# Kernel optimization log

Measured on AMD Instinct MI355X. Metric: run time of the kernel, lower is better.

## Reference

```python
import jax, jax.numpy as jnp
import numpy as np

N = 50000      # nodes
E = 800000     # edges (avg degree 16)
B = 8          # graphs in batch
H = 128        # hidden (message_passer out_channels)
FF = 64        # fourier_feat_dim -> fourier features have dim 2*FF
REPEATS = 4    # repeats_training
OUT = 4        # output_dim
IN_X = 5
IN_MASK = 3

def _fourier(x, M):
    # https://arxiv.org/pdf/2106.02795.pdf : [cos(xM), sin(xM)] / sqrt(2F)
    p = x @ M
    return jnp.concatenate([jnp.cos(p), jnp.sin(p)], axis=-1) / jnp.sqrt(2.0 * M.shape[1])

def _seg_mean(v, idx, n):
    s = jax.ops.segment_sum(v, idx, num_segments=n)
    c = jax.ops.segment_sum(jnp.ones((v.shape[0],), v.dtype), idx, num_segments=n)
    return s / jnp.maximum(c, 1.0)[:, None]

def setup_inputs() -> dict:
    key = jax.random.key(0)
    ks = jax.random.split(key, 16)
    x = jax.random.normal(ks[0], (N, IN_X), jnp.float32)
    x_mask = jax.random.bernoulli(ks[1], 0.1, (N, IN_MASK)).astype(jnp.float32)
    edge_index = jax.random.randint(ks[2], (2, E), 0, N)
    edge_attr = jax.random.normal(ks[3], (E, 3), jnp.float32)
    pos = jax.random.uniform(ks[4], (N, 2), jnp.float32)
    batch = jnp.sort(jax.random.randint(ks[5], (N,), 0, B))
    sampling_points = jax.random.uniform(ks[6], (2,), jnp.float32)
    fourier_mat = jax.random.normal(ks[7], (2, FF), jnp.float32)  # learnable, init N(0,1)
    W_enc = jax.random.normal(ks[8], (IN_X + IN_MASK, H), jnp.float32) * 0.1
    b_enc = jnp.zeros((H,), jnp.float32)
    W_msg = jax.random.normal(ks[9], (2 * H + 3, H), jnp.float32) * 0.05
    b_msg = jnp.zeros((H,), jnp.float32)
    W_upd = jax.random.normal(ks[10], (4 * H, H), jnp.float32) * 0.05
    b_upd = jnp.zeros((H,), jnp.float32)
    W_dec = jax.random.normal(ks[11], (H, OUT), jnp.float32) * 0.1
    b_dec = jnp.zeros((OUT,), jnp.float32)
    return dict(x=x, x_mask=x_mask, edge_index=edge_index, edge_attr=edge_attr,
                pos=pos, batch=batch, sampling_points=sampling_points,
                fourier_mat=fourier_mat, W_enc=W_enc, b_enc=b_enc,
                W_msg=W_msg, b_msg=b_msg, W_upd=W_upd, b_upd=b_upd,
                W_dec=W_dec, b_dec=b_dec)

def reference(x, x_mask, edge_index, edge_attr, pos, batch, sampling_points,
              fourier_mat, W_enc, b_enc, W_msg, b_msg, W_upd, b_upd, W_dec, b_dec):
    bc = x_mask[:, -1]                                   # 0/1 BC flag
    x_full = jnp.concatenate([x, x_mask], axis=1)        # x = concat([x, x_mask])
    keys_ff = _fourier(pos, fourier_mat)                 # input fourier features [N, 2F]
    h = jax.nn.relu(x_full @ W_enc + b_enc)              # encoder -> [N, H]

    # x_BC: scatter-mean over BC nodes per graph (computed once)
    bc_sum = jax.ops.segment_sum(h * bc[:, None], batch, num_segments=B)
    bc_cnt = jax.ops.segment_sum(bc, batch, num_segments=B)
    x_BC = bc_sum / jnp.maximum(bc_cnt, 1.0)[:, None]    # [B, H]

    x_graph = _seg_mean(h, batch, B)                     # global_mean_pool [B, H]
    src, dst = edge_index[0], edge_index[1]
    deg = jnp.maximum(jax.ops.segment_sum(jnp.ones((E,), h.dtype), dst, num_segments=N), 1.0)

    for _ in range(REPEATS):  # repeated message passing
        m = jax.nn.relu(jnp.concatenate([h[src], h[dst], edge_attr], axis=1) @ W_msg + b_msg)
        agg = jax.ops.segment_sum(m, dst, num_segments=N) / deg[:, None]  # scatter-mean
        upd_in = jnp.concatenate([h, agg, x_graph[batch], x_BC[batch]], axis=1)
        h = h + jax.nn.relu(upd_in @ W_upd + b_upd)
        x_graph = _seg_mean(h, batch, B)                 # re-pool each repeat

    decoded = h @ W_dec + b_dec                          # [N, OUT]

    # kernelized fourier-feature interpolation at the sampling point
    q = _fourier(sampling_points, fourier_mat)           # [2F]
    nq = q / jnp.linalg.norm(q)
    nk = keys_ff / jnp.linalg.norm(keys_ff, axis=1, keepdims=True)
    vals_sum = h.sum(axis=0)                             # [H]
    kwv = nk.T @ h                                       # [2F, H]
    ks_sum = nk.sum(axis=0)                              # [2F]
    enc = (vals_sum + nq @ kwv) / (N + nq @ ks_sum)      # [H]
    U_sampled = enc @ W_dec + b_dec                      # [OUT]
    # pack (U_sampled, decoded) into one array: row 0 = sampled point, rows 1: = nodes
    return jnp.concatenate([U_sampled[None, :], decoded], axis=0)
```

## Files before the change

### kernel.cpp

```cpp
#include <hip/hip_runtime.h>
#include <math.h>

#define Nn 50000
#define Ee 800000
#define Bb 8
#define ROUNDS 4
#define KWVB 512
#define SCB 196
#define AP 40
#define HP 132
#define KS 40
#define NBK 196
#define P1B 391
#define CHUNK 2047

typedef __attribute__((ext_vector_type(8))) short bf16x8;
typedef __attribute__((ext_vector_type(4))) float f32x4;

__device__ inline short f2bf(float f) {
  union { float f; unsigned u; } v; v.f = f;
  unsigned r = v.u + 0x7fff + ((v.u >> 16) & 1);
  return (short)(r >> 16);
}
__device__ inline float bf2f(short s) {
  union { float f; unsigned u; } v; v.u = ((unsigned)(unsigned short)s) << 16;
  return v.f;
}

__global__ __launch_bounds__(256) void encode_seg(
    const float* __restrict__ x, const float* __restrict__ xm,
    const int* __restrict__ batch, const float* __restrict__ W,
    const float* __restrict__ b, float* __restrict__ h,
    float* __restrict__ gsum, float* __restrict__ gcnt,
    float* __restrict__ bcsum, float* __restrict__ bccnt) {
  __shared__ float xs5[128 * 5];
  __shared__ float xm3[128 * 3];
  __shared__ float ls[Bb * 128];
  __shared__ float lb[Bb * 128];
  __shared__ float lc[Bb], lbc[Bb];
  const int t = threadIdx.x;
  const int nBase = blockIdx.x * 128;
  const int j = t & 127, half = t >> 7;
  const int base5 = nBase * 5, base3 = nBase * 3;
  for (int q = t; q < 640; q += 256) xs5[q] = (base5 + q < Nn * 5) ? x[base5 + q] : 0.f;
  for (int q = t; q < 384; q += 256) xm3[q] = (base3 + q < Nn * 3) ? xm[base3 + q] : 0.f;
  for (int q = t; q < Bb * 128; q += 256) { ls[q] = 0.f; lb[q] = 0.f; }
  if (t < Bb) { lc[t] = 0.f; lbc[t] = 0.f; }
  float Wcol[8];
#pragma unroll
  for (int k = 0; k < 8; k++) Wcol[k] = W[k * 128 + j];
  const float bj = b[j];
  __syncthreads();
  int curb = -1;
  float runh = 0.f, runb = 0.f, runc = 0.f, runbc = 0.f;
  for (int kk = 0; kk < 64; kk++) {
    int i = nBase + kk * 2 + half;
    if (i >= Nn) break;
    int li = i - nBase;
    float acc = bj;
#pragma unroll
    for (int k = 0; k < 5; k++) acc = fmaf(xs5[li * 5 + k], Wcol[k], acc);
#pragma unroll
    for (int k = 0; k < 3; k++) acc = fmaf(xm3[li * 3 + k], Wcol[5 + k], acc);
    float v = fmaxf(acc, 0.f);
    h[(size_t)i * 128 + j] = v;
    float bc = xm3[li * 3 + 2];
    int g = batch[i];
    if (g != curb) {
      if (curb >= 0) {
        atomicAdd(&ls[curb * 128 + j], runh);
        atomicAdd(&lb[curb * 128 + j], runb);
        if (j == 0) { atomicAdd(&lc[curb], runc); atomicAdd(&lbc[curb], runbc); }
      }
      curb = g; runh = runb = runc = runbc = 0.f;
    }
    runh += v; runb += v * bc;
    if (j == 0) { runc += 1.f; runbc += bc; }
  }
  if (curb >= 0) {
    atomicAdd(&ls[curb * 128 + j], runh);
    atomicAdd(&lb[curb * 128 + j], runb);
    if (j == 0) { atomicAdd(&lc[curb], runc); atomicAdd(&lbc[curb], runbc); }
  }
  __syncthreads();
  for (int q = t; q < Bb * 128; q += 256) {
    float a = ls[q], c = lb[q];
    if (a != 0.f) atomicAdd(&gsum[q], a);
    if (c != 0.f) atomicAdd(&bcsum[q], c);
  }
  if (t < Bb) { atomicAdd(&gcnt[t], lc[t]); atomicAdd(&bccnt[t], lbc[t]); }
}

__global__ __launch_bounds__(256) void split_w_kernel(
    const float* __restrict__ Wm, const float* __restrict__ Wu,
    short* __restrict__ Wmt_h, short* __restrict__ Wmt_l,
    short* __restrict__ Wut_h, short* __restrict__ Wut_l) {
  int idx = blockIdx.x * 256 + threadIdx.x;
  if (idx < 32768) {
    int k = idx & 127, n = (idx >> 7) & 127, y = idx >> 14;
    float w = Wm[(size_t)(y * 128 + k) * 128 + n];
    short hi = f2bf(w);
    Wmt_h[idx] = hi;
    Wmt_l[idx] = f2bf(w - bf2f(hi));
  } else if (idx < 65536) {
    int j = idx - 32768;
    int k = j & 255, n = j >> 8;
    float w = Wu[(size_t)k * 128 + n];
    short hi = f2bf(w);
    Wut_h[j] = hi;
    Wut_l[j] = f2bf(w - bf2f(hi));
  }
}

__global__ __launch_bounds__(256) void bkt_cnt(const int* __restrict__ ei,
                                               int* __restrict__ bktcnt) {
  __shared__ int hist[NBK];
  int t = threadIdx.x;
  for (int q = t; q < NBK; q += 256) hist[q] = 0;
  __syncthreads();
  int base = blockIdx.x * CHUNK;
  int end = base + CHUNK < Ee ? base + CHUNK : Ee;
  for (int e = base + t; e < end; e += 256) atomicAdd(&hist[ei[Ee + e] >> 8], 1);
  __syncthreads();
  for (int q = t; q < NBK; q += 256)
    if (hist[q]) atomicAdd(&bktcnt[q], hist[q]);
}
__global__ __launch_bounds__(256) void bkt_scan(const int* __restrict__ bktcnt,
                                                int* __restrict__ bktbase,
                                                int* __restrict__ bktcur) {
  __shared__ int s[256];
  int t = threadIdx.x;
  int v = (t < NBK) ? bktcnt[t] : 0;
  s[t] = v;
  __syncthreads();
  for (int off = 1; off < 256; off <<= 1) {
    int x = (t >= off) ? s[t - off] : 0;
    __syncthreads();
    s[t] += x;
    __syncthreads();
  }
  int ex = s[t] - v;
  if (t < NBK) { bktbase[t] = ex; bktcur[t] = ex; }
  if (t == NBK - 1) bktbase[NBK] = ex + v;
}
__global__ __launch_bounds__(256) void bkt_part(
    const int* __restrict__ ei, const float* __restrict__ ea,
    int* __restrict__ bktcur, int2* __restrict__ recA,
    unsigned char* __restrict__ dlo) {
  __shared__ int hist[NBK], lbase[NBK], lcur[NBK];
  int t = threadIdx.x;
  for (int q = t; q < NBK; q += 256) hist[q] = 0;
  __syncthreads();
  int base = blockIdx.x * CHUNK;
  int end = base + CHUNK < Ee ? base + CHUNK : Ee;
  for (int e = base + t; e < end; e += 256) atomicAdd(&hist[ei[Ee + e] >> 8], 1);
  __syncthreads();
  for (int q = t; q < NBK; q += 256) {
    int c = hist[q];
    lbase[q] = c ? atomicAdd(&bktcur[q], c) : 0;
    lcur[q] = 0;
  }
  __syncthreads();
  for (int e = base + t; e < end; e += 256) {
    int d = ei[Ee + e];
    int bk = d >> 8;
    int p = lbase[bk] + atomicAdd(&lcur[bk], 1);
    unsigned r0 = (unsigned)ei[e] |
                  ((unsigned)(unsigned short)f2bf(ea[3 * (size_t)e + 0]) << 16);
    unsigned r1 = (unsigned)(unsigned short)f2bf(ea[3 * (size_t)e + 1]) |
                  ((unsigned)(unsigned short)f2bf(ea[3 * (size_t)e + 2]) << 16);
    recA[p] = make_int2((int)r0, (int)r1);
    dlo[p] = (unsigned char)(d & 255);
  }
}
__global__ __launch_bounds__(256) void dst_cnt(const int* __restrict__ bktbase,
                                               const unsigned char* __restrict__ dlo,
                                               int* __restrict__ cnt) {
  __shared__ int hh[256];
  int t = threadIdx.x;
  hh[t] = 0;
  __syncthreads();
  int b = blockIdx.x;
  int lo = bktbase[b], hi = bktbase[b + 1];
  for (int i = lo + t; i < hi; i += 256) atomicAdd(&hh[dlo[i]], 1);
  __syncthreads();
  int d = b * 256 + t;
  if (d < Nn) cnt[d] = hh[t];
}
__global__ __launch_bounds__(256) void bsum_kernel(const int* __restrict__ cnt,
                                                   int* __restrict__ bsum) {
  __shared__ int wsum[4];
  int t = threadIdx.x;
  int i = blockIdx.x * 256 + t;
  int v = (i < Nn) ? cnt[i] : 0;
#pragma unroll
  for (int off = 32; off > 0; off >>= 1) v += __shfl_down(v, off);
  if ((t & 63) == 0) wsum[t >> 6] = v;
  __syncthreads();
  if (t == 0) bsum[blockIdx.x] = wsum[0] + wsum[1] + wsum[2] + wsum[3];
}
__global__ __launch_bounds__(256) void scan_top_kernel(const int* __restrict__ bsum,
                                                       int* __restrict__ boff) {
  __shared__ int s[256];
  int t = threadIdx.x;
  int v = (t < SCB) ? bsum[t] : 0;
  s[t] = v;
  __syncthreads();
  for (int off = 1; off < 256; off <<= 1) {
    int x = (t >= off) ? s[t - off] : 0;
    __syncthreads();
    s[t] += x;
    __syncthreads();
  }
  boff[t] = s[t] - v;
}
__global__ __launch_bounds__(256) void apply_kernel(
    const int* __restrict__ cnt, const int* __restrict__ boff,
    int* __restrict__ rowptr, float* __restrict__ invdeg) {
  __shared__ int s[256];
  int t = threadIdx.x;
  int i = blockIdx.x * 256 + t;
  int v = (i < Nn) ? cnt[i] : 0;
  s[t] = v;
  __syncthreads();
  for (int off = 1; off < 256; off <<= 1) {
    int x = (t >= off) ? s[t - off] : 0;
    __syncthreads();
    s[t] += x;
    __syncthreads();
  }
  int ex = boff[blockIdx.x] + s[t] - v;
  if (i < Nn) {
    rowptr[i] = ex;
    invdeg[i] = 1.0f / fmaxf((float)v, 1.0f);
    if (i == Nn - 1) rowptr[Nn] = ex + v;
  }
}
__global__ __launch_bounds__(256) void bkt_fin(
    const int* __restrict__ bktbase, const int2* __restrict__ recA,
    const unsigned char* __restrict__ dlo, const int* __restrict__ rowptr,
    int2* __restrict__ rec) {
  __shared__ int cur[256];
  int t = threadIdx.x;
  int b = blockIdx.x;
  int d = b * 256 + t;
  cur[t] = (d < Nn) ? rowptr[d] : 0;
  __syncthreads();
  int lo = bktbase[b], hi = bktbase[b + 1];
  for (int i = lo + t; i < hi; i += 256) {
    int dl = dlo[i];
    int p = atomicAdd(&cur[dl], 1);
    rec[p] = recA[i];
  }
}

__global__ __launch_bounds__(128) void gb_static_kernel(
    const float* __restrict__ bcsum, const float* __restrict__ bccnt,
    const float* __restrict__ Wu, const float* __restrict__ bu,
    float* __restrict__ gbst) {
  __shared__ float xb[128];
  int g = blockIdx.x, t = threadIdx.x;
  xb[t] = bcsum[g * 128 + t] / fmaxf(bccnt[g], 1.f);
  __syncthreads();
  float acc = bu[t];
#pragma unroll 4
  for (int k = 0; k < 128; k++) acc = fmaf(xb[k], Wu[(size_t)(384 + k) * 128 + t], acc);
  gbst[g * 128 + t] = acc;
}

__global__ __launch_bounds__(128) void gb_dyn_kernel(
    const float* __restrict__ gsum, const float* __restrict__ gcnt,
    const float* __restrict__ gbst, const float* __restrict__ Wu,
    float* __restrict__ gb) {
  __shared__ float xg[128];
  int g = blockIdx.x, t = threadIdx.x;
  xg[t] = gsum[g * 128 + t] / fmaxf(gcnt[g], 1.f);
  __syncthreads();
  float acc = gbst[g * 128 + t];
#pragma unroll 4
  for (int k = 0; k < 128; k++) acc = fmaf(xg[k], Wu[(size_t)(256 + k) * 128 + t], acc);
  gb[g * 128 + t] = acc;
}

__global__ __launch_bounds__(256) void proj_mfma(
    const float* __restrict__ h, const short* __restrict__ Wth,
    const short* __restrict__ Wtl, unsigned char* __restrict__ hs8,
    unsigned short* __restrict__ hdbf) {
  __shared__ short Ah_s[128 * AP], Al_s[128 * AP];
  __shared__ short Bh_s[128 * AP], Bl_s[128 * AP];
  const int t = threadIdx.x;
  const int nBase = blockIdx.x * 128;
  const int yoff = blockIdx.y * 16384;
  const int wave = t >> 6, lane = t & 63;
  const int ml = lane & 15, quad = lane >> 4;
  const int ko = quad * 8;

  f32x4 acc[2][8];
#pragma unroll
  for (int nt = 0; nt < 2; nt++)
#pragma unroll
    for (int mt = 0; mt < 8; mt++)
#pragma unroll
      for (int q = 0; q < 4; q++) acc[nt][mt][q] = 0.f;

  const int srow = t >> 1;
  const int kc = (t & 1) * 16;
  const int nd0 = nBase + srow;
  const int nn = nd0 < Nn ? nd0 : Nn - 1;

  for (int c = 0; c < 4; c++) {
    const float* p = &h[(size_t)nn * 128 + c * 32 + kc];
    float4 u0 = *(const float4*)(p + 0);
    float4 u1 = *(const float4*)(p + 4);
    float4 u2 = *(const float4*)(p + 8);
    float4 u3 = *(const float4*)(p + 12);
    const int k0 = c * 32;
    const bf16x8 gb0 = *(const bf16x8*)&Wth[(size_t)yoff + srow * 128 + k0 + kc];
    const bf16x8 gb1 = *(const bf16x8*)&Wth[(size_t)yoff + srow * 128 + k0 + kc + 8];
    const bf16x8 gl0 = *(const bf16x8*)&Wtl[(size_t)yoff + srow * 128 + k0 + kc];
    const bf16x8 gl1 = *(const bf16x8*)&Wtl[(size_t)yoff + srow * 128 + k0 + kc + 8];
    float xs[16] = {u0.x,u0.y,u0.z,u0.w, u1.x,u1.y,u1.z,u1.w,
                    u2.x,u2.y,u2.z,u2.w, u3.x,u3.y,u3.z,u3.w};
    bf16x8 vh0, vh1, vl0, vl1;
#pragma unroll
    for (int j = 0; j < 8; j++) {
      short hi = f2bf(xs[j]);
      vh0[j] = hi; vl0[j] = f2bf(xs[j] - bf2f(hi));
    }
#pragma unroll
    for (int j = 0; j < 8; j++) {
      short hi = f2bf(xs[8 + j]);
      vh1[j] = hi; vl1[j] = f2bf(xs[8 + j] - bf2f(hi));
    }
    __syncthreads();
    *(bf16x8*)&Ah_s[srow * AP + kc] = vh0;
    *(bf16x8*)&Ah_s[srow * AP + kc + 8] = vh1;
    *(bf16x8*)&Al_s[srow * AP + kc] = vl0;
    *(bf16x8*)&Al_s[srow * AP + kc + 8] = vl1;
    *(bf16x8*)&Bh_s[srow * AP + kc] = gb0;
    *(bf16x8*)&Bh_s[srow * AP + kc + 8] = gb1;
    *(bf16x8*)&Bl_s[srow * AP + kc] = gl0;
    *(bf16x8*)&Bl_s[srow * AP + kc + 8] = gl1;
    __syncthreads();
#pragma unroll
    for (int mt = 0; mt < 8; mt++) {
      const int ar = (mt * 16 + ml) * AP + ko;
      bf16x8 ah = *(const bf16x8*)&Ah_s[ar];
      bf16x8 al = *(const bf16x8*)&Al_s[ar];
#pragma unroll
      for (int nt = 0; nt < 2; nt++) {
        const int br = (wave * 32 + nt * 16 + ml) * AP + ko;
        bf16x8 bh = *(const bf16x8*)&Bh_s[br];
        bf16x8 bl = *(const bf16x8*)&Bl_s[br];
        acc[nt][mt] = __builtin_amdgcn_mfma_f32_16x16x32_bf16(ah, bh, acc[nt][mt], 0, 0, 0);
        acc[nt][mt] = __builtin_amdgcn_mfma_f32_16x16x32_bf16(ah, bl, acc[nt][mt], 0, 0, 0);
        acc[nt][mt] = __builtin_amdgcn_mfma_f32_16x16x32_bf16(al, bh, acc[nt][mt], 0, 0, 0);
      }
    }
  }
  if (blockIdx.y == 0) {
#pragma unroll
    for (int nt = 0; nt < 2; nt++) {
      const int ch = wave * 32 + nt * 16 + ml;
#pragma unroll
      for (int mt = 0; mt < 8; mt++) {
#pragma unroll
        for (int q = 0; q < 4; q++) {
          int nd = nBase + mt * 16 + quad * 4 + q;
          if (nd < Nn) {
            int pk = __builtin_amdgcn_cvt_pk_fp8_f32(acc[nt][mt][q], acc[nt][mt][q], 0, false);
            hs8[(size_t)nd * 128 + ch] = (unsigned char)(pk & 0xff);
          }
        }
      }
    }
  } else {
#pragma unroll
    for (int nt = 0; nt < 2; nt++) {
      const int ch = wave * 32 + nt * 16 + ml;
#pragma unroll
      for (int mt = 0; mt < 8; mt++) {
#pragma unroll
        for (int q = 0; q < 4; q++) {
          int nd = nBase + mt * 16 + quad * 4 + q;
          if (nd < Nn) hdbf[(size_t)nd * 128 + ch] = (unsigned short)f2bf(acc[nt][mt][q]);
        }
      }
    }
  }
}

__global__ __launch_bounds__(256) void agg_kernel(
    const unsigned char* __restrict__ hs8, const unsigned short* __restrict__ hdbf,
    unsigned short* __restrict__ aggbf, const int2* __restrict__ rec,
    const int* __restrict__ rowptr, const float* __restrict__ invdeg,
    const float* __restrict__ Wm, const float* __restrict__ bm) {
  int t = threadIdx.x;
  int hw = t >> 5, lane = t & 31;
  int v = blockIdx.x * 8 + hw;
  if (v >= Nn) return;
  int c0 = lane * 4;
  const float4 We0 = *(const float4*)&Wm[(size_t)256 * 128 + c0];
  const float4 We1 = *(const float4*)&Wm[(size_t)257 * 128 + c0];
  const float4 We2 = *(const float4*)&Wm[(size_t)258 * 128 + c0];
  const float4 b4  = *(const float4*)&bm[c0];
  const ushort4 hd4 = *(const ushort4*)&hdbf[(size_t)v * 128 + c0];
  const float bx = b4.x + bf2f((short)hd4.x), by = b4.y + bf2f((short)hd4.y),
              bz = b4.z + bf2f((short)hd4.z), bw = b4.w + bf2f((short)hd4.w);
  float ax = 0.f, ay = 0.f, az = 0.f, aw = 0.f;
  float ax2 = 0.f, ay2 = 0.f, az2 = 0.f, aw2 = 0.f;
  const int r0 = rowptr[v], r1 = rowptr[v + 1];
  int e = r0;
  for (; e + 2 <= r1; e += 2) {
    int2 q0 = rec[e], q1 = rec[e + 1];
    int s0 = q0.x & 0xffff, s1 = q1.x & 0xffff;
    unsigned hr0 = *(const unsigned*)&hs8[(size_t)s0 * 128 + c0];
    unsigned hr1 = *(const unsigned*)&hs8[(size_t)s1 * 128 + c0];
    float e00 = bf2f((short)(q0.x >> 16));
    float e01 = bf2f((short)(q0.y & 0xffff));
    float e02 = bf2f((short)(q0.y >> 16));
    float e10 = bf2f((short)(q1.x >> 16));
    float e11 = bf2f((short)(q1.y & 0xffff));
    float e12 = bf2f((short)(q1.y >> 16));
    float h0x = __builtin_amdgcn_cvt_f32_fp8(hr0, 0);
    float h0y = __builtin_amdgcn_cvt_f32_fp8(hr0, 1);
    float h0z = __builtin_amdgcn_cvt_f32_fp8(hr0, 2);
    float h0w = __builtin_amdgcn_cvt_f32_fp8(hr0, 3);
    float h1x = __builtin_amdgcn_cvt_f32_fp8(hr1, 0);
    float h1y = __builtin_amdgcn_cvt_f32_fp8(hr1, 1);
    float h1z = __builtin_amdgcn_cvt_f32_fp8(hr1, 2);
    float h1w = __builtin_amdgcn_cvt_f32_fp8(hr1, 3);
    ax += fmaxf(fmaf(e00, We0.x, fmaf(e01, We1.x, fmaf(e02, We2.x, h0x + bx))), 0.f);
    ay += fmaxf(fmaf(e00, We0.y, fmaf(e01, We1.y, fmaf(e02, We2.y, h0y + by))), 0.f);
    az += fmaxf(fmaf(e00, We0.z, fmaf(e01, We1.z, fmaf(e02, We2.z, h0z + bz))), 0.f);
    aw += fmaxf(fmaf(e00, We0.w, fmaf(e01, We1.w, fmaf(e02, We2.w, h0w + bw))), 0.f);
    ax2 += fmaxf(fmaf(e10, We0.x, fmaf(e11, We1.x, fmaf(e12, We2.x, h1x + bx))), 0.f);
    ay2 += fmaxf(fmaf(e10, We0.y, fmaf(e11, We1.y, fmaf(e12, We2.y, h1y + by))), 0.f);
    az2 += fmaxf(fmaf(e10, We0.z, fmaf(e11, We1.z, fmaf(e12, We2.z, h1z + bz))), 0.f);
    aw2 += fmaxf(fmaf(e10, We0.w, fmaf(e11, We1.w, fmaf(e12, We2.w, h1w + bw))), 0.f);
  }
  if (e < r1) {
    int2 q0 = rec[e];
    int s0 = q0.x & 0xffff;
    unsigned hr0 = *(const unsigned*)&hs8[(size_t)s0 * 128 + c0];
    float e00 = bf2f((short)(q0.x >> 16));
    float e01 = bf2f((short)(q0.y & 0xffff));
    float e02 = bf2f((short)(q0.y >> 16));
    float h0x = __builtin_amdgcn_cvt_f32_fp8(hr0, 0);
    float h0y = __builtin_amdgcn_cvt_f32_fp8(hr0, 1);
    float h0z = __builtin_amdgcn_cvt_f32_fp8(hr0, 2);
    float h0w = __builtin_amdgcn_cvt_f32_fp8(hr0, 3);
    ax += fmaxf(fmaf(e00, We0.x, fmaf(e01, We1.x, fmaf(e02, We2.x, h0x + bx))), 0.f);
    ay += fmaxf(fmaf(e00, We0.y, fmaf(e01, We1.y, fmaf(e02, We2.y, h0y + by))), 0.f);
    az += fmaxf(fmaf(e00, We0.z, fmaf(e01, We1.z, fmaf(e02, We2.z, h0z + bz))), 0.f);
    aw += fmaxf(fmaf(e00, We0.w, fmaf(e01, We1.w, fmaf(e02, We2.w, h0w + bw))), 0.f);
  }
  const float idg = invdeg[v];
  ushort4 o;
  o.x = (unsigned short)f2bf((ax + ax2) * idg);
  o.y = (unsigned short)f2bf((ay + ay2) * idg);
  o.z = (unsigned short)f2bf((az + az2) * idg);
  o.w = (unsigned short)f2bf((aw + aw2) * idg);
  *(ushort4*)&aggbf[(size_t)v * 128 + c0] = o;
}

__global__ __launch_bounds__(256) void updg_mfma(
    float* __restrict__ h, const unsigned short* __restrict__ aggbf,
    const int* __restrict__ batch,
    const short* __restrict__ Wth, const short* __restrict__ Wtl,
    const float* __restrict__ gb, float* __restrict__ gsum_out) {
  __shared__ short Ah_s[128 * AP], Al_s[128 * AP];
  __shared__ short Bh_s[128 * AP], Bl_s[128 * AP];
  __shared__ float gbs[Bb * 128];
  __shared__ float ls[Bb * 128];
  const int t = threadIdx.x;
  const int nBase = blockIdx.x * 128;
  *(float4*)&gbs[t * 4] = *(const float4*)&gb[t * 4];
#pragma unroll
  for (int q = 0; q < 4; q++) ls[t + q * 256] = 0.f;

  const int wave = t >> 6, lane = t & 63;
  const int ml = lane & 15, quad = lane >> 4;
  const int ko = quad * 8;

  f32x4 acc[2][8];
#pragma unroll
  for (int nt = 0; nt < 2; nt++)
#pragma unroll
    for (int mt = 0; mt < 8; mt++)
#pragma unroll
      for (int q = 0; q < 4; q++) acc[nt][mt][q] = 0.f;

  const int srow = t >> 1;
  const int kc = (t & 1) * 16;
  const int nd0 = nBase + srow;
  const int nn = nd0 < Nn ? nd0 : Nn - 1;

  for (int c = 0; c < 8; c++) {
    const int k0 = c * 32;
    bf16x8 vh0, vh1, vl0, vl1;
    if (c < 4) {
      const float* p = &h[(size_t)nn * 128 + c * 32 + kc];
      float4 u0 = *(const float4*)(p + 0);
      float4 u1 = *(const float4*)(p + 4);
      float4 u2 = *(const float4*)(p + 8);
      float4 u3 = *(const float4*)(p + 12);
      float xs[16] = {u0.x,u0.y,u0.z,u0.w, u1.x,u1.y,u1.z,u1.w,
                      u2.x,u2.y,u2.z,u2.w, u3.x,u3.y,u3.z,u3.w};
#pragma unroll
      for (int j = 0; j < 8; j++) {
        short hi = f2bf(xs[j]);
        vh0[j] = hi; vl0[j] = f2bf(xs[j] - bf2f(hi));
      }
#pragma unroll
      for (int j = 0; j < 8; j++) {
        short hi = f2bf(xs[8 + j]);
        vh1[j] = hi; vl1[j] = f2bf(xs[8 + j] - bf2f(hi));
      }
    } else {
      const unsigned short* pa = &aggbf[(size_t)nn * 128 + (c - 4) * 32 + kc];
      vh0 = *(const bf16x8*)(pa);
      vh1 = *(const bf16x8*)(pa + 8);
    }
    const bf16x8 gb0 = *(const bf16x8*)&Wth[(size_t)srow * 256 + k0 + kc];
    const bf16x8 gb1 = *(const bf16x8*)&Wth[(size_t)srow * 256 + k0 + kc + 8];
    const bf16x8 gl0 = *(const bf16x8*)&Wtl[(size_t)srow * 256 + k0 + kc];
    const bf16x8 gl1 = *(const bf16x8*)&Wtl[(size_t)srow * 256 + k0 + kc + 8];
    __syncthreads();
    *(bf16x8*)&Ah_s[srow * AP + kc] = vh0;
    *(bf16x8*)&Ah_s[srow * AP + kc + 8] = vh1;
    if (c < 4) {
      *(bf16x8*)&Al_s[srow * AP + kc] = vl0;
      *(bf16x8*)&Al_s[srow * AP + kc + 8] = vl1;
    }
    *(bf16x8*)&Bh_s[srow * AP + kc] = gb0;
    *(bf16x8*)&Bh_s[srow * AP + kc + 8] = gb1;
    *(bf16x8*)&Bl_s[srow * AP + kc] = gl0;
    *(bf16x8*)&Bl_s[srow * AP + kc + 8] = gl1;
    __syncthreads();
    if (c < 4) {
#pragma unroll
      for (int mt = 0; mt < 8; mt++) {
        const int ar = (mt * 16 + ml) * AP + ko;
        bf16x8 ah = *(const bf16x8*)&Ah_s[ar];
        bf16x8 al = *(const bf16x8*)&Al_s[ar];
#pragma unroll
        for (int nt = 0; nt < 2; nt++) {
          const int br = (wave * 32 + nt * 16 + ml) * AP + ko;
          bf16x8 bh = *(const bf16x8*)&Bh_s[br];
          bf16x8 bl = *(const bf16x8*)&Bl_s[br];
          acc[nt][mt] = __builtin_amdgcn_mfma_f32_16x16x32_bf16(ah, bh, acc[nt][mt], 0, 0, 0);
          acc[nt][mt] = __builtin_amdgcn_mfma_f32_16x16x32_bf16(ah, bl, acc[nt][mt], 0, 0, 0);
          acc[nt][mt] = __builtin_amdgcn_mfma_f32_16x16x32_bf16(al, bh, acc[nt][mt], 0, 0, 0);
        }
      }
    } else {
#pragma unroll
      for (int mt = 0; mt < 8; mt++) {
        const int ar = (mt * 16 + ml) * AP + ko;
        bf16x8 ah = *(const bf16x8*)&Ah_s[ar];
#pragma unroll
        for (int nt = 0; nt < 2; nt++) {
          const int br = (wave * 32 + nt * 16 + ml) * AP + ko;
          bf16x8 bh = *(const bf16x8*)&Bh_s[br];
          bf16x8 bl = *(const bf16x8*)&Bl_s[br];
          acc[nt][mt] = __builtin_amdgcn_mfma_f32_16x16x32_bf16(ah, bh, acc[nt][mt], 0, 0, 0);
          acc[nt][mt] = __builtin_amdgcn_mfma_f32_16x16x32_bf16(ah, bl, acc[nt][mt], 0, 0, 0);
        }
      }
    }
  }
#pragma unroll
  for (int nt = 0; nt < 2; nt++) {
    const int ch = wave * 32 + nt * 16 + ml;
#pragma unroll
    for (int mt = 0; mt < 8; mt++) {
      int rbase = nBase + mt * 16 + quad * 4;
      float runv = 0.f;
      int curb = -1;
#pragma unroll
      for (int q = 0; q < 4; q++) {
        int nd = rbase + q;
        if (nd < Nn) {
          int bi = batch[nd];
          float u = fmaxf(acc[nt][mt][q] + gbs[bi * 128 + ch], 0.f);
          float hn = h[(size_t)nd * 128 + ch] + u;
          h[(size_t)nd * 128 + ch] = hn;
          if (bi != curb) {
            if (curb >= 0) atomicAdd(&ls[curb * 128 + ch], runv);
            curb = bi;
            runv = 0.f;
          }
          runv += hn;
        }
      }
      if (curb >= 0) atomicAdd(&ls[curb * 128 + ch], runv);
    }
  }
  __syncthreads();
#pragma unroll
  for (int q = 0; q < 4; q++) {
    int idx = t + q * 256;
    float v = ls[idx];
    if (v != 0.f) atomicAdd(&gsum_out[idx], v);
  }
}

__global__ __launch_bounds__(256) void kwv_kernel(
    const float* __restrict__ h, const float* __restrict__ pos,
    const float* __restrict__ Fm, const float* __restrict__ Wd,
    const float* __restrict__ bd, float* __restrict__ partial,
    float* __restrict__ ksum, float* __restrict__ out) {
  __shared__ float h_s[32 * HP];
  __shared__ short nkT[128 * KS];
  __shared__ short hT[128 * KS];
  __shared__ float wd[512];
  __shared__ float ksum_s[128];
  const int t = threadIdx.x;
  const int hr = t >> 3;
  const int hc = (t & 7) * 16;
  const int fg = (t & 7) * 8;
  const int wave = t >> 6, lane = t & 63;
  const int ml = lane & 15, quad = lane >> 4;
  const int ko = quad * 8;
  if (t < 128) { *(float4*)&wd[t * 4] = *(const float4*)&Wd[t * 4]; ksum_s[t] = 0.f; }
  const float bdv = bd[t & 3];
  f32x4 acc[2][8];
#pragma unroll
  for (int nt = 0; nt < 2; nt++)
#pragma unroll
    for (int mt = 0; mt < 8; mt++)
#pragma unroll
      for (int q = 0; q < 4; q++) acc[nt][mt][q] = 0.f;
  float klc[8], kls[8];
#pragma unroll
  for (int f = 0; f < 8; f++) { klc[f] = 0.f; kls[f] = 0.f; }

  const int nTiles = (Nn + 31) / 32;
  for (int tile = blockIdx.x; tile < nTiles; tile += gridDim.x) {
    const int gh = tile * 32 + hr;
    float4 hv0 = {0.f, 0.f, 0.f, 0.f}, hv1 = hv0, hv2 = hv0, hv3 = hv0;
    float cbuf[8], sbuf[8];
    if (gh < Nn) {
      const float* hp = &h[(size_t)gh * 128 + hc];
      hv0 = *(const float4*)(hp + 0);
      hv1 = *(const float4*)(hp + 4);
      hv2 = *(const float4*)(hp + 8);
      hv3 = *(const float4*)(hp + 12);
      const float px = pos[gh * 2 + 0], py = pos[gh * 2 + 1];
#pragma unroll
      for (int f = 0; f < 8; f++) {
        float p = px * Fm[fg + f] + py * Fm[64 + fg + f];
        cbuf[f] = cosf(p) * 0.125f;
        sbuf[f] = sinf(p) * 0.125f;
      }
    } else {
#pragma unroll
      for (int f = 0; f < 8; f++) { cbuf[f] = 0.f; sbuf[f] = 0.f; }
    }
    float xs[16] = {hv0.x,hv0.y,hv0.z,hv0.w, hv1.x,hv1.y,hv1.z,hv1.w,
                    hv2.x,hv2.y,hv2.z,hv2.w, hv3.x,hv3.y,hv3.z,hv3.w};
    __syncthreads();
    *(float4*)&h_s[hr * HP + hc + 0]  = hv0;
    *(float4*)&h_s[hr * HP + hc + 4]  = hv1;
    *(float4*)&h_s[hr * HP + hc + 8]  = hv2;
    *(float4*)&h_s[hr * HP + hc + 12] = hv3;
#pragma unroll
    for (int i = 0; i < 16; i++) hT[(hc + i) * KS + hr] = f2bf(xs[i]);
#pragma unroll
    for (int f = 0; f < 8; f++) {
      nkT[(fg + f) * KS + hr] = f2bf(cbuf[f]);
      nkT[(64 + fg + f) * KS + hr] = f2bf(sbuf[f]);
      klc[f] += cbuf[f];
      kls[f] += sbuf[f];
    }
    __syncthreads();
#pragma unroll
    for (int mt = 0; mt < 8; mt++) {
      bf16x8 ah = *(const bf16x8*)&nkT[(mt * 16 + ml) * KS + ko];
#pragma unroll
      for (int nt = 0; nt < 2; nt++) {
        bf16x8 bh = *(const bf16x8*)&hT[(wave * 32 + nt * 16 + ml) * KS + ko];
        acc[nt][mt] = __builtin_amdgcn_mfma_f32_16x16x32_bf16(ah, bh, acc[nt][mt], 0, 0, 0);
      }
    }
    if (t < 128) {
      int n = t >> 2, o = t & 3;
      int gn = tile * 32 + n;
      if (gn < Nn) {
        float s = bdv;
#pragma unroll 4
        for (int kk = 0; kk < 128; kk++) {
          int k = (kk + n) & 127;
          s = fmaf(h_s[n * HP + k], wd[k * 4 + o], s);
        }
        out[4 + (size_t)gn * 4 + o] = s;
      }
    }
  }
  float* pb = &partial[(size_t)blockIdx.x * 16384];
#pragma unroll
  for (int nt = 0; nt < 2; nt++) {
    const int col = wave * 32 + nt * 16 + ml;
#pragma unroll
    for (int mt = 0; mt < 8; mt++) {
#pragma unroll
      for (int q = 0; q < 4; q++) {
        int row = mt * 16 + quad * 4 + q;
        pb[row * 128 + col] = acc[nt][mt][q];
      }
    }
  }
#pragma unroll
  for (int f = 0; f < 8; f++) {
    atomicAdd(&ksum_s[fg + f], klc[f]);
    atomicAdd(&ksum_s[64 + fg + f], kls[f]);
  }
  __syncthreads();
  if (t < 128) atomicAdd(&ksum[t], ksum_s[t]);
}

__global__ __launch_bounds__(256) void kwv_reduce(const float* __restrict__ partial,
                                                  float* __restrict__ kwv) {
  int idx = blockIdx.x * 256 + threadIdx.x;
  float s = 0.f;
  for (int b = 0; b < KWVB; b++) s += partial[(size_t)b * 16384 + idx];
  kwv[idx] = s;
}

__global__ __launch_bounds__(128) void final_kernel(
    const float* __restrict__ sp, const float* __restrict__ Fm,
    const float* __restrict__ kwv, const float* __restrict__ vs,
    const float* __restrict__ ksum, const float* __restrict__ Wd,
    const float* __restrict__ bd, float* __restrict__ out) {
  __shared__ float nq_s[128];
  __shared__ float red[2];
  __shared__ float redU[8];
  int t = threadIdx.x;
  int jj = t & 63;
  float p = sp[0] * Fm[jj] + sp[1] * Fm[64 + jj];
  nq_s[t] = ((t < 64) ? cosf(p) : sinf(p)) * 0.125f;
  __syncthreads();
  float num = 0.f;
#pragma unroll
  for (int g = 0; g < Bb; g++) num += vs[g * 128 + t];
  for (int k = 0; k < 128; k++) num = fmaf(nq_s[k], kwv[k * 128 + t], num);
  float dp = nq_s[t] * ksum[t];
#pragma unroll
  for (int off = 32; off > 0; off >>= 1) dp += __shfl_down(dp, off);
  if ((t & 63) == 0) red[t >> 6] = dp;
  __syncthreads();
  float den = (float)Nn + red[0] + red[1];
  float e = num / den;
  float u[4];
#pragma unroll
  for (int o = 0; o < 4; o++) u[o] = e * Wd[t * 4 + o];
#pragma unroll
  for (int off = 32; off > 0; off >>= 1) {
#pragma unroll
    for (int o = 0; o < 4; o++) u[o] += __shfl_down(u[o], off);
  }
  if ((t & 63) == 0) {
#pragma unroll
    for (int o = 0; o < 4; o++) redU[(t >> 6) * 4 + o] = u[o];
  }
  __syncthreads();
  if (t < 4) out[t] = redU[t] + redU[4 + t] + bd[t];
}

extern "C" void kernel_launch(void* const* d_in, const int* in_sizes, int n_in,
                              void* d_out, int out_size, void* d_ws, size_t ws_size,
                              hipStream_t stream) {
  const float* x    = (const float*)d_in[0];
  const float* xm   = (const float*)d_in[1];
  const int*   ei   = (const int*)d_in[2];
  const float* ea   = (const float*)d_in[3];
  const float* pos  = (const float*)d_in[4];
  const int*   batch= (const int*)d_in[5];
  const float* sp   = (const float*)d_in[6];
  const float* Fm   = (const float*)d_in[7];
  const float* Wenc = (const float*)d_in[8];
  const float* benc = (const float*)d_in[9];
  const float* Wmsg = (const float*)d_in[10];
  const float* bmsg = (const float*)d_in[11];
  const float* Wupd = (const float*)d_in[12];
  const float* bupd = (const float*)d_in[13];
  const float* Wdec = (const float*)d_in[14];
  const float* bdec = (const float*)d_in[15];
  float* out = (float*)d_out;

  float* ws     = (float*)d_ws;
  float* h      = ws;
  float* agg    = h + (size_t)Nn * 128;
  float* aux    = agg + (size_t)Nn * 128;
  float* invdeg = aux + (size_t)Nn * 128;
  float* gsum   = invdeg + Nn;
  float* gcnt   = gsum + 1024;
  float* bcsum  = gcnt + 8;
  float* bccnt  = bcsum + 1024;
  float* gsumR  = bccnt + 8;
  float* vsum   = gsumR + 4096;
  float* ksum   = vsum + 128;
  float* gbst   = ksum + 128;
  float* gbuf   = gbst + 1024;
  float* kwv    = gbuf + 4096;
  int2*  rec    = (int2*)(kwv + 16384);
  int*   cnt    = (int*)(rec + Ee);
  int*   rowptr = cnt + Nn;
  int*   bsum   = rowptr + Nn + 1;
  int*   boff   = bsum + 256;
  int*   bktcnt = boff + 256;
  int*   bktbase= bktcnt + 196;
  int*   bktcur = bktbase + 197;
  short* wmt_h  = (short*)(bktcur + 196);
  short* wmt_l  = wmt_h + 32768;
  short* wut_h  = wmt_l + 32768;
  short* wut_l  = wut_h + 32768;
  int2*  recA   = (int2*)(wut_l + 32768);
  unsigned char* dlo = (unsigned char*)(recA + Ee);

  unsigned short* aggbf = (unsigned short*)agg;
  unsigned char*  hs8   = (unsigned char*)aux;
  unsigned short* hdbf  = (unsigned short*)(hs8 + (size_t)Nn * 128);

  hipMemsetAsync(gsum, 0, 6416 * sizeof(float), stream);
  hipMemsetAsync(bktcnt, 0, 196 * sizeof(int), stream);

  split_w_kernel<<<256, 256, 0, stream>>>(Wmsg, Wupd, wmt_h, wmt_l, wut_h, wut_l);

  bkt_cnt<<<P1B, 256, 0, stream>>>(ei, bktcnt);
  bkt_scan<<<1, 256, 0, stream>>>(bktcnt, bktbase, bktcur);
  bkt_part<<<P1B, 256, 0, stream>>>(ei, ea, bktcur, recA, dlo);
  dst_cnt<<<NBK, 256, 0, stream>>>(bktbase, dlo, cnt);
  bsum_kernel<<<SCB, 256, 0, stream>>>(cnt, bsum);
  scan_top_kernel<<<1, 256, 0, stream>>>(bsum, boff);
  apply_kernel<<<SCB, 256, 0, stream>>>(cnt, boff, rowptr, invdeg);
  bkt_fin<<<NBK, 256, 0, stream>>>(bktbase, recA, dlo, rowptr, rec);

  const int nb128 = (Nn + 127) / 128;
  encode_seg<<<nb128, 256, 0, stream>>>(x, xm, batch, Wenc, benc, h,
                                        gsum, gcnt, bcsum, bccnt);
  gb_static_kernel<<<Bb, 128, 0, stream>>>(bcsum, bccnt, Wupd, bupd, gbst);
  gb_dyn_kernel<<<Bb, 128, 0, stream>>>(gsum, gcnt, gbst, Wupd, gbuf);

  for (int r = 0; r < ROUNDS; r++) {
    proj_mfma<<<dim3(nb128, 2), 256, 0, stream>>>(h, wmt_h, wmt_l, hs8, hdbf);
    agg_kernel<<<(Nn + 7) / 8, 256, 0, stream>>>(hs8, hdbf, aggbf, rec, rowptr,
                                                 invdeg, Wmsg, bmsg);
    updg_mfma<<<nb128, 256, 0, stream>>>(h, aggbf, batch, wut_h, wut_l,
                                         gbuf + r * 1024, gsumR + r * 1024);
    if (r < ROUNDS - 1)
      gb_dyn_kernel<<<Bb, 128, 0, stream>>>(gsumR + r * 1024, gcnt, gbst, Wupd,
                                            gbuf + (r + 1) * 1024);
  }

  kwv_kernel<<<KWVB, 256, 0, stream>>>(h, pos, Fm, Wdec, bdec, agg, ksum, out);
  kwv_reduce<<<64, 256, 0, stream>>>(agg, kwv);
  final_kernel<<<1, 128, 0, stream>>>(sp, Fm, kwv, gsumR + 3 * 1024, ksum,
                                      Wdec, bdec, out);
}
```

Measured before the change: 708.8 us.

## Drop split-bf16 compensation in message projection and spread decoder work across all threads

The message projection GEMM now uses a single bf16 MFMA per tile instead of three hi/lo compensated products, so it stops building and storing the low-part operands in shared memory. This cuts the MFMA count and LDS traffic about threefold, at the cost of lower precision in the projected features, which are later stored as fp8/bf16 anyway. Separately, the decoder dot product in the kwv kernel is now split across all 256 threads, each doing half the K range. The partial sums go through shared memory and are combined and written at the next tile's barrier, which removes the idle half-block.

```diff
diff --git a/kernel.cpp b/kernel.cpp
--- a/kernel.cpp
+++ b/kernel.cpp
@@ -284,10 +284,9 @@
 
 __global__ __launch_bounds__(256) void proj_mfma(
     const float* __restrict__ h, const short* __restrict__ Wth,
-    const short* __restrict__ Wtl, unsigned char* __restrict__ hs8,
-    unsigned short* __restrict__ hdbf) {
-  __shared__ short Ah_s[128 * AP], Al_s[128 * AP];
-  __shared__ short Bh_s[128 * AP], Bl_s[128 * AP];
+    unsigned char* __restrict__ hs8, unsigned short* __restrict__ hdbf) {
+  __shared__ short Ah_s[128 * AP];
+  __shared__ short Bh_s[128 * AP];
   const int t = threadIdx.x;
   const int nBase = blockIdx.x * 128;
   const int yoff = blockIdx.y * 16384;
@@ -317,44 +316,28 @@
     const int k0 = c * 32;
     const bf16x8 gb0 = *(const bf16x8*)&Wth[(size_t)yoff + srow * 128 + k0 + kc];
     const bf16x8 gb1 = *(const bf16x8*)&Wth[(size_t)yoff + srow * 128 + k0 + kc + 8];
-    const bf16x8 gl0 = *(const bf16x8*)&Wtl[(size_t)yoff + srow * 128 + k0 + kc];
-    const bf16x8 gl1 = *(const bf16x8*)&Wtl[(size_t)yoff + srow * 128 + k0 + kc + 8];
     float xs[16] = {u0.x,u0.y,u0.z,u0.w, u1.x,u1.y,u1.z,u1.w,
                     u2.x,u2.y,u2.z,u2.w, u3.x,u3.y,u3.z,u3.w};
-    bf16x8 vh0, vh1, vl0, vl1;
-#pragma unroll
-    for (int j = 0; j < 8; j++) {
-      short hi = f2bf(xs[j]);
-      vh0[j] = hi; vl0[j] = f2bf(xs[j] - bf2f(hi));
-    }
-#pragma unroll
-    for (int j = 0; j < 8; j++) {
-      short hi = f2bf(xs[8 + j]);
-      vh1[j] = hi; vl1[j] = f2bf(xs[8 + j] - bf2f(hi));
-    }
+    bf16x8 vh0, vh1;
+#pragma unroll
+    for (int j = 0; j < 8; j++) vh0[j] = f2bf(xs[j]);
+#pragma unroll
+    for (int j = 0; j < 8; j++) vh1[j] = f2bf(xs[8 + j]);
     __syncthreads();
     *(bf16x8*)&Ah_s[srow * AP + kc] = vh0;
     *(bf16x8*)&Ah_s[srow * AP + kc + 8] = vh1;
-    *(bf16x8*)&Al_s[srow * AP + kc] = vl0;
-    *(bf16x8*)&Al_s[srow * AP + kc + 8] = vl1;
     *(bf16x8*)&Bh_s[srow * AP + kc] = gb0;
     *(bf16x8*)&Bh_s[srow * AP + kc + 8] = gb1;
-    *(bf16x8*)&Bl_s[srow * AP + kc] = gl0;
-    *(bf16x8*)&Bl_s[srow * AP + kc + 8] = gl1;
     __syncthreads();
 #pragma unroll
     for (int mt = 0; mt < 8; mt++) {
       const int ar = (mt * 16 + ml) * AP + ko;
       bf16x8 ah = *(const bf16x8*)&Ah_s[ar];
-      bf16x8 al = *(const bf16x8*)&Al_s[ar];
 #pragma unroll
       for (int nt = 0; nt < 2; nt++) {
         const int br = (wave * 32 + nt * 16 + ml) * AP + ko;
         bf16x8 bh = *(const bf16x8*)&Bh_s[br];
-        bf16x8 bl = *(const bf16x8*)&Bl_s[br];
         acc[nt][mt] = __builtin_amdgcn_mfma_f32_16x16x32_bf16(ah, bh, acc[nt][mt], 0, 0, 0);
-        acc[nt][mt] = __builtin_amdgcn_mfma_f32_16x16x32_bf16(ah, bl, acc[nt][mt], 0, 0, 0);
-        acc[nt][mt] = __builtin_amdgcn_mfma_f32_16x16x32_bf16(al, bh, acc[nt][mt], 0, 0, 0);
       }
     }
   }
@@ -616,6 +599,7 @@
   __shared__ short hT[128 * KS];
   __shared__ float wd[512];
   __shared__ float ksum_s[128];
+  __shared__ float dsum[256];
   const int t = threadIdx.x;
   const int hr = t >> 3;
   const int hc = (t & 7) * 16;
@@ -625,6 +609,8 @@
   const int ko = quad * 8;
   if (t < 128) { *(float4*)&wd[t * 4] = *(const float4*)&Wd[t * 4]; ksum_s[t] = 0.f; }
   const float bdv = bd[t & 3];
+  const int dn = (t & 127) >> 2, dno = t & 3;
+  const int dk0 = (t >> 7) * 64;
   f32x4 acc[2][8];
 #pragma unroll
   for (int nt = 0; nt < 2; nt++)
@@ -636,6 +622,7 @@
 #pragma unroll
   for (int f = 0; f < 8; f++) { klc[f] = 0.f; kls[f] = 0.f; }
 
+  int ptile = -1;
   const int nTiles = (Nn + 31) / 32;
   for (int tile = blockIdx.x; tile < nTiles; tile += gridDim.x) {
     const int gh = tile * 32 + hr;
@@ -661,6 +648,10 @@
     float xs[16] = {hv0.x,hv0.y,hv0.z,hv0.w, hv1.x,hv1.y,hv1.z,hv1.w,
                     hv2.x,hv2.y,hv2.z,hv2.w, hv3.x,hv3.y,hv3.z,hv3.w};
     __syncthreads();
+    if (ptile >= 0 && t < 128) {
+      int gn = ptile * 32 + dn;
+      if (gn < Nn) out[4 + (size_t)gn * 4 + dno] = dsum[t] + dsum[t + 128] + bdv;
+    }
     *(float4*)&h_s[hr * HP + hc + 0]  = hv0;
     *(float4*)&h_s[hr * HP + hc + 4]  = hv1;
     *(float4*)&h_s[hr * HP + hc + 8]  = hv2;
@@ -684,19 +675,21 @@
         acc[nt][mt] = __builtin_amdgcn_mfma_f32_16x16x32_bf16(ah, bh, acc[nt][mt], 0, 0, 0);
       }
     }
-    if (t < 128) {
-      int n = t >> 2, o = t & 3;
-      int gn = tile * 32 + n;
-      if (gn < Nn) {
-        float s = bdv;
+    {
+      float s = 0.f;
 #pragma unroll 4
-        for (int kk = 0; kk < 128; kk++) {
-          int k = (kk + n) & 127;
-          s = fmaf(h_s[n * HP + k], wd[k * 4 + o], s);
-        }
-        out[4 + (size_t)gn * 4 + o] = s;
-      }
-    }
+      for (int kk = dk0; kk < dk0 + 64; kk++) {
+        int k = (kk + dn) & 127;
+        s = fmaf(h_s[dn * HP + k], wd[k * 4 + dno], s);
+      }
+      dsum[t] = s;
+    }
+    ptile = tile;
+  }
+  __syncthreads();
+  if (ptile >= 0 && t < 128) {
+    int gn = ptile * 32 + dn;
+    if (gn < Nn) out[4 + (size_t)gn * 4 + dno] = dsum[t] + dsum[t + 128] + bdv;
   }
   float* pb = &partial[(size_t)blockIdx.x * 16384];
 #pragma unroll
@@ -844,7 +837,7 @@
   gb_dyn_kernel<<<Bb, 128, 0, stream>>>(gsum, gcnt, gbst, Wupd, gbuf);
 
   for (int r = 0; r < ROUNDS; r++) {
-    proj_mfma<<<dim3(nb128, 2), 256, 0, stream>>>(h, wmt_h, wmt_l, hs8, hdbf);
+    proj_mfma<<<dim3(nb128, 2), 256, 0, stream>>>(h, wmt_h, hs8, hdbf);
     agg_kernel<<<(Nn + 7) / 8, 256, 0, stream>>>(hs8, hdbf, aggbf, rec, rowptr,
                                                  invdeg, Wmsg, bmsg);
     updg_mfma<<<nb128, 256, 0, stream>>>(h, aggbf, batch, wut_h, wut_l,
```

Result: faster. 675.1 us (-4.8%).
